# Kernel tuning notes

Measured on AMD Instinct MI355X. Metric: run time of the kernel, lower is better.

The kernel has to match this reference:

```python
import jax, jax.numpy as jnp
import numpy as np
import math

B, L, D = 4, 4096, 1024
PI = math.pi
LN_EPS = 1e-5


def setup_inputs() -> dict:
    key = jax.random.key(0)
    ks = jax.random.split(key, 16)
    s = 1.0 / math.sqrt(D)
    inp = {
        "x": jax.random.normal(ks[0], (B, L, D), dtype=jnp.float32),
        # Linear weights stored as [in, out] (torch W.T)
        "Wk": jax.random.normal(ks[1], (D, D), dtype=jnp.float32) * s,
        "bk": jnp.zeros((D,), dtype=jnp.float32),
        "Wq": jax.random.normal(ks[2], (D, D), dtype=jnp.float32) * s,
        "bq": jnp.zeros((D,), dtype=jnp.float32),
        "Wv": jax.random.normal(ks[3], (D, D), dtype=jnp.float32) * s,
        "bv": jnp.zeros((D,), dtype=jnp.float32),
        "ln_g": jnp.ones((D,), dtype=jnp.float32),
        "ln_b": jnp.zeros((D,), dtype=jnp.float32),
        "Wo": jax.random.normal(ks[4], (D, D), dtype=jnp.float32) * s,
        "bo": jnp.zeros((D,), dtype=jnp.float32),
        "Wg1": jax.random.normal(ks[5], (D, D // 4), dtype=jnp.float32) * s,
        "bg1": jnp.zeros((D // 4,), dtype=jnp.float32),
        "Wg2": jax.random.normal(ks[6], (D // 4, 1), dtype=jnp.float32) * (2.0 / math.sqrt(D)),
        "bg2": jnp.zeros((1,), dtype=jnp.float32),
        "pos_phases": jax.random.normal(ks[7], (L, D), dtype=jnp.float32) * PI,
    }
    return inp


def _layernorm(x, g, b):
    mu = jnp.mean(x, axis=-1, keepdims=True)
    var = jnp.var(x, axis=-1, keepdims=True)
    return (x - mu) * jax.lax.rsqrt(var + LN_EPS) * g + b


def reference(x, Wk, bk, Wq, bq, Wv, bv, ln_g, ln_b, Wo, bo, Wg1, bg1, Wg2, bg2, pos_phases):
    # dropout is identity in eval mode
    key_phases = jnp.tanh(x @ Wk + bk) * PI          # [B,L,D]
    query_phases = jnp.tanh(x @ Wq + bq) * PI        # [B,L,D]
    V = x @ Wv + bv                                   # [B,L,D]

    cos_k, sin_k = jnp.cos(key_phases), jnp.sin(key_phases)
    cos_q, sin_q = jnp.cos(query_phases), jnp.sin(query_phases)

    mem_real = jnp.cumsum(V * cos_k, axis=1)
    mem_imag = jnp.cumsum(V * sin_k, axis=1)
    content_retrieved = mem_real * cos_q + mem_imag * sin_q

    pp = pos_phases[: x.shape[1]]                     # [L,D]
    cos_p, sin_p = jnp.cos(pp), jnp.sin(pp)
    pos_mem_real = jnp.cumsum(V * cos_p, axis=1)
    pos_mem_imag = jnp.cumsum(V * sin_p, axis=1)
    pos_retrieved = pos_mem_real * cos_p + pos_mem_imag * sin_p

    gate = jax.nn.sigmoid(jax.nn.gelu(x @ Wg1 + bg1) @ Wg2 + bg2)  # [B,L,1]
    combined = gate * content_retrieved + (1.0 - gate) * pos_retrieved

    positions = jnp.arange(1, x.shape[1] + 1, dtype=jnp.float32)
    norm = jnp.sqrt(positions)[None, :, None]
    out = _layernorm(combined / norm, ln_g, ln_b) @ Wo + bo
    return x + out
```

## Files before the change

kernel.cpp:

```cpp
#include <hip/hip_runtime.h>
#include <math.h>

#define B_ 4
#define L_ 4096
#define D_ 1024
#define DG_ 256
#define NC_ 128
#define CL_ 32
#define SEGL_ 8
#define NSEG_ 16
#define PI_F 3.14159265358979323846f
#define LN_EPS_F 1e-5f

typedef __attribute__((ext_vector_type(8))) _Float16 f16x8;
typedef __attribute__((ext_vector_type(8))) short s16x8;
typedef __attribute__((ext_vector_type(4))) short s16x4;
typedef __attribute__((ext_vector_type(4))) float f32x4;

__device__ inline short f2h(float f) { return __builtin_bit_cast(short, (_Float16)f); }
__device__ inline float h2f(short s) { return (float)__builtin_bit_cast(_Float16, s); }

__device__ inline float ftanh(float x) {
    float e = __expf(2.0f * x);
    return 1.0f - 2.0f / (e + 1.0f);
}
__device__ inline void fsincos(float x, float* s, float* c) {
    *s = __sinf(x); *c = __cosf(x);
}

__device__ inline void gld16(const void* g, void* l) {
    __builtin_amdgcn_global_load_lds(
        (const __attribute__((address_space(1))) unsigned int*)g,
        (__attribute__((address_space(3))) unsigned int*)l, 16, 0, 0);
}

__global__ __launch_bounds__(256)
void conv_x(const float* __restrict__ x, short* __restrict__ xh, int n8)
{
    int t = blockIdx.x * 256 + threadIdx.x;
    if (t >= n8) return;
    const float4* p = (const float4*)x + (size_t)t * 2;
    float4 a = p[0], b = p[1];
    s16x8 v;
    v[0] = f2h(a.x); v[1] = f2h(a.y); v[2] = f2h(a.z); v[3] = f2h(a.w);
    v[4] = f2h(b.x); v[5] = f2h(b.y); v[6] = f2h(b.z); v[7] = f2h(b.w);
    *(s16x8*)(xh + (size_t)t * 8) = v;
}

__global__ __launch_bounds__(256)
void csp_kernel(const float* __restrict__ PP, short* __restrict__ CSP, int n4)
{
    int t = blockIdx.x * 256 + threadIdx.x;
    if (t >= n4) return;
    f32x4 p = *(const f32x4*)&PP[(size_t)t * 4];
    s16x8 o;
    #pragma unroll
    for (int j = 0; j < 4; ++j) {
        float s, c;
        fsincos(p[j], &s, &c);
        o[2 * j] = f2h(c);
        o[2 * j + 1] = f2h(s);
    }
    *(s16x8*)&CSP[(size_t)t * 8] = o;
}

__global__ __launch_bounds__(256)
void convT(const float* __restrict__ W, short* __restrict__ Th, int N)
{
    __shared__ float tile[64][65];
    const int n0 = blockIdx.x * 64, k0 = blockIdx.y * 64;
    const int t = threadIdx.x;
    const int r = t >> 4, c4 = (t & 15) * 4;

    #pragma unroll
    for (int i = 0; i < 4; ++i) {
        float4 v = *(const float4*)&W[(size_t)(k0 + r + i * 16) * N + n0 + c4];
        tile[r + i * 16][c4 + 0] = v.x;
        tile[r + i * 16][c4 + 1] = v.y;
        tile[r + i * 16][c4 + 2] = v.z;
        tile[r + i * 16][c4 + 3] = v.w;
    }
    __syncthreads();
    #pragma unroll
    for (int i = 0; i < 4; ++i) {
        const int n = r + i * 16;
        s16x4 o;
        o[0] = f2h(tile[c4 + 0][n]);
        o[1] = f2h(tile[c4 + 1][n]);
        o[2] = f2h(tile[c4 + 2][n]);
        o[3] = f2h(tile[c4 + 3][n]);
        *(s16x4*)&Th[(size_t)(n0 + n) * 1024 + k0 + c4] = o;
    }
}

#define BARRIER() __builtin_amdgcn_s_barrier()
#define PRIO1() __builtin_amdgcn_s_setprio(1)
#define PRIO0() __builtin_amdgcn_s_setprio(0)
#define LGKM0() do { asm volatile("s_waitcnt lgkmcnt(0)" ::: "memory"); \
                     __builtin_amdgcn_sched_barrier(0); } while (0)
#define VMC(N) asm volatile("s_waitcnt vmcnt(" #N ")" ::: "memory")

#define DSR(dst, areg, OFS)                                              \
    asm volatile("ds_read_b128 %0, %1 offset:" OFS                       \
                 : "=v"(dst) : "v"(areg))

#define RDA4(areg)                                                       \
    DSR(af[0], areg, "0");    DSR(af[1], areg, "2048");                  \
    DSR(af[2], areg, "4096"); DSR(af[3], areg, "6144");
#define RDA4H(areg)                                                      \
    DSR(af[0], areg, "8192");  DSR(af[1], areg, "10240");                \
    DSR(af[2], areg, "12288"); DSR(af[3], areg, "14336");
#define RDB4(areg, KK)                                                   \
    DSR(bq[0][KK], areg, "0");    DSR(bq[1][KK], areg, "2048");          \
    DSR(bq[2][KK], areg, "4096"); DSR(bq[3][KK], areg, "6144");

#define MF(MG, KK)                                                       \
    _Pragma("unroll") for (int i_ = 0; i_ < 4; ++i_)                     \
    _Pragma("unroll") for (int n_ = 0; n_ < 4; ++n_)                     \
        acc[(MG)*4 + i_][n_] = __builtin_amdgcn_mfma_f32_16x16x32_f16(   \
            af[i_], bq[n_][KK], acc[(MG)*4 + i_][n_], 0, 0, 0);

template<int EPI, typename OT>
__global__ __launch_bounds__(512, 2)
void mgemm256(const short* __restrict__ A, const short* __restrict__ Bt,
              const float* __restrict__ X, OT* __restrict__ out0,
              short* __restrict__ out1, short* __restrict__ out2,
              const float* __restrict__ b0, const float* __restrict__ b1,
              const float* __restrict__ b2, int M, int N, int K)
{
    extern __shared__ char lds[];

    const int tid = threadIdx.x;
    const int w = tid >> 6, l = tid & 63;
    const int wr = w >> 2, wc = w & 3;
    const int fr = l & 15, kb = l >> 4;
    const int bm = blockIdx.x * 256, bn = blockIdx.y * 256;
    const int np = K >> 7;

    const int s = fr & 7;
    const int cK0 = (((s >> 2) & 1) << 6) | (((kb ^ s) & 3) << 4);
    const int aA0 = (wr << 14) + fr * 128 + cK0;
    const int aA1 = aA0 ^ 64;
    const int aB0 = 32768 + ((wc >> 1) << 14) + ((wc & 1) * 64 + fr) * 128 + cK0;
    const int aB1 = aB0 ^ 64;
    const int aA0o = aA0 + 65536, aA1o = aA1 + 65536;
    const int aB0o = aB0 + 65536, aB1o = aB1 + 65536;

    const int p0 = tid * 16;
    const int sr = p0 >> 7;
    const int sc = (p0 & 127) ^ ((sr & 7) << 4);
    const short* gA = A  + (size_t)(bm + sr) * K + (sc >> 1);
    const short* gB = Bt + (size_t)(bn + sr) * K + (sc >> 1);
    char* ldst = lds + (w << 10);
    const size_t q1 = (size_t)64 * K, q2 = 2 * q1, q3 = 3 * q1;

    f32x4 acc[8][4] = {};
    f16x8 af[4];
    f16x8 bq[4][2];

    gld16(gA,      ldst);          gld16(gA + q1, ldst + 8192);
    gld16(gA + q2, ldst + 16384);  gld16(gA + q3, ldst + 24576);
    gld16(gB,      ldst + 32768);  gld16(gB + q1, ldst + 40960);
    gld16(gB + q2, ldst + 49152);  gld16(gB + q3, ldst + 57344);
    gld16(gA +      64, ldst + 65536);
    gld16(gA + q2 + 64, ldst + 65536 + 16384);
    VMC(2);
    BARRIER();

    const short* gAn = gA + 64;
    const short* gBn = gB + 64;

    for (int pp = 0; pp < np; ++pp) {
        const bool nl = (pp + 1 < np);

        RDA4(aA0); RDB4(aB0, 0);
        gld16(gBn,      ldst + 98304);
        gld16(gBn + q1, ldst + 98304 + 8192);
        LGKM0();
        PRIO1(); MF(0, 0); PRIO0();
        RDA4(aA1); RDB4(aB1, 1);
        gld16(gBn + q2, ldst + 98304 + 16384);
        gld16(gBn + q3, ldst + 98304 + 24576);
        gld16(gAn + q1, ldst + 65536 + 8192);
        gld16(gAn + q3, ldst + 65536 + 24576);
        LGKM0();
        PRIO1(); MF(0, 1); PRIO0();
        BARRIER();
        RDA4H(aA0);
        LGKM0();
        PRIO1(); MF(1, 0); PRIO0();
        RDA4H(aA1);
        if (nl) { gld16(gAn + 64, ldst); gld16(gAn + 64 + q2, ldst + 16384); }
        LGKM0();
        PRIO1(); MF(1, 1); PRIO0();
        if (nl) { VMC(2); } else { VMC(0); }
        BARRIER();

        RDA4(aA0o); RDB4(aB0o, 0);
        if (nl) {
            gld16(gBn +      64, ldst + 32768);
            gld16(gBn + q1 + 64, ldst + 40960);
        }
        LGKM0();
        PRIO1(); MF(0, 0); PRIO0();
        RDA4(aA1o); RDB4(aB1o, 1);
        if (nl) {
            gld16(gBn + q2 + 64, ldst + 49152);
            gld16(gBn + q3 + 64, ldst + 57344);
            gld16(gAn + q1 + 64, ldst + 8192);
            gld16(gAn + q3 + 64, ldst + 24576);
        }
        LGKM0();
        PRIO1(); MF(0, 1); PRIO0();
        BARRIER();
        RDA4H(aA0o);
        LGKM0();
        PRIO1(); MF(1, 0); PRIO0();
        RDA4H(aA1o);
        if (nl) { gld16(gAn + 128, ldst + 65536); gld16(gAn + 128 + q2, ldst + 65536 + 16384); }
        LGKM0();
        PRIO1(); MF(1, 1); PRIO0();
        if (nl) {
            VMC(2);
            BARRIER();
        }
        gAn += 128; gBn += 128;
    }

    if constexpr (EPI == 4) {
        short* op; const float* bp; bool dt;
        if (bn < 1024)      { op = (short*)out0; bp = b0; dt = true;  }
        else if (bn < 2048) { op = out1;         bp = b1; dt = true;  }
        else                { op = out2;         bp = b2; dt = false; }
        const int cb = bn & 1023;
        float bc[4];
        #pragma unroll
        for (int nf = 0; nf < 4; ++nf) bc[nf] = bp[cb + wc * 64 + nf * 16 + fr];
        #pragma unroll
        for (int mf = 0; mf < 8; ++mf)
            #pragma unroll
            for (int rr = 0; rr < 4; ++rr) {
                const int row = bm + wr * 128 + mf * 16 + kb * 4 + rr;
                #pragma unroll
                for (int nf = 0; nf < 4; ++nf) {
                    const int cc = cb + wc * 64 + nf * 16 + fr;
                    float c = acc[mf][nf][rr] + bc[nf];
                    if (dt) c = ftanh(c) * PI_F;
                    op[(size_t)row * 1024 + cc] = f2h(c);
                }
            }
    } else {
        float bc[4];
        #pragma unroll
        for (int nf = 0; nf < 4; ++nf) bc[nf] = b0[bn + wc * 64 + nf * 16 + fr];
        #pragma unroll
        for (int mf = 0; mf < 8; ++mf)
            #pragma unroll
            for (int rr = 0; rr < 4; ++rr) {
                const int row = bm + wr * 128 + mf * 16 + kb * 4 + rr;
                #pragma unroll
                for (int nf = 0; nf < 4; ++nf) {
                    const int col = bn + wc * 64 + nf * 16 + fr;
                    float c = acc[mf][nf][rr] + bc[nf] + X[(size_t)row * N + col];
                    ((float*)out0)[(size_t)row * N + col] = c;
                }
            }
    }
}

#define RDAF(areg)                                                       \
    DSR(af[0], areg, "0");    DSR(af[1], areg, "2048");                  \
    DSR(af[2], areg, "4096"); DSR(af[3], areg, "6144");
#define RDBF(areg)                                                       \
    DSR(bqs[0], areg, "0");    DSR(bqs[1], areg, "2048");                \
    DSR(bqs[2], areg, "4096"); DSR(bqs[3], areg, "6144");

#define MF16()                                                           \
    _Pragma("unroll") for (int i_ = 0; i_ < 4; ++i_)                     \
    _Pragma("unroll") for (int n_ = 0; n_ < 4; ++n_)                     \
        acc[i_][n_] = __builtin_amdgcn_mfma_f32_16x16x32_f16(            \
            af[i_], bqs[n_], acc[i_][n_], 0, 0, 0);

template<int EPI>
__global__ __launch_bounds__(256, 2)
void gemm128(const short* __restrict__ A, const short* __restrict__ Bt,
             const float* __restrict__ b0, const float* __restrict__ wg2p,
             float* __restrict__ gatep, int M, int N, int K)
{
    extern __shared__ char lds[];

    const int tid = threadIdx.x;
    const int w = tid >> 6, l = tid & 63;
    const int wr = w >> 1, wc = w & 1;
    const int fr = l & 15, kb = l >> 4;
    const int bm = blockIdx.x * 128, bn = blockIdx.y * 128;

    const int s = fr & 7;
    const int cK0 = (((s >> 2) & 1) << 6) | (((kb ^ s) & 3) << 4);
    const int aA0e = (wr * 64 + fr) * 128 + cK0;
    const int aA1e = aA0e ^ 64;
    const int aB0e = 16384 + (wc * 64 + fr) * 128 + cK0;
    const int aB1e = aB0e ^ 64;
    const int aA0o = aA0e + 32768, aA1o = aA1e + 32768;
    const int aB0o = aB0e + 32768, aB1o = aB1e + 32768;

    const int p16 = tid * 16;
    const int sr = p16 >> 7;
    const int sc = (p16 & 127) ^ ((sr & 7) << 4);
    const short* gA = A  + (size_t)(bm + sr) * K + (sc >> 1);
    const short* gB = Bt + (size_t)(bn + sr) * K + (sc >> 1);
    char* ldA = lds + (w << 10);
    const size_t r32 = (size_t)32 * K;

    f32x4 acc[4][4] = {};
    f16x8 af[4], bqs[4];

    #pragma unroll
    for (int i = 0; i < 4; ++i) gld16(gA + i * r32, ldA + i * 4096);
    #pragma unroll
    for (int i = 0; i < 4; ++i) gld16(gB + i * r32, ldA + 16384 + i * 4096);
    VMC(0);
    BARRIER();

    const short* gAt = gA;
    const short* gBt = gB;
    const int np = K >> 7;

    for (int pp = 0; pp < np; ++pp) {
        const bool nl = (pp + 1 < np);

        RDAF(aA0e); RDBF(aB0e);
        #pragma unroll
        for (int i = 0; i < 4; ++i) gld16(gAt + 64 + i * r32, ldA + 32768 + i * 4096);
        LGKM0();
        PRIO1(); MF16(); PRIO0();
        RDAF(aA1e); RDBF(aB1e);
        #pragma unroll
        for (int i = 0; i < 4; ++i) gld16(gBt + 64 + i * r32, ldA + 49152 + i * 4096);
        LGKM0();
        PRIO1(); MF16(); PRIO0();
        VMC(0);
        BARRIER();

        RDAF(aA0o); RDBF(aB0o);
        if (nl) {
            #pragma unroll
            for (int i = 0; i < 4; ++i) gld16(gAt + 128 + i * r32, ldA + i * 4096);
        }
        LGKM0();
        PRIO1(); MF16(); PRIO0();
        RDAF(aA1o); RDBF(aB1o);
        if (nl) {
            #pragma unroll
            for (int i = 0; i < 4; ++i) gld16(gBt + 128 + i * r32, ldA + 16384 + i * 4096);
        }
        LGKM0();
        PRIO1(); MF16(); PRIO0();
        if (nl) {
            VMC(0);
            BARRIER();
        }
        gAt += 128; gBt += 128;
    }

    float bg[4], wg[4];
    #pragma unroll
    for (int nf = 0; nf < 4; ++nf) {
        const int cl = bn + wc * 64 + nf * 16 + fr;
        bg[nf] = b0[cl];
        wg[nf] = wg2p[cl];
    }
    #pragma unroll
    for (int mf = 0; mf < 4; ++mf)
        #pragma unroll
        for (int rr = 0; rr < 4; ++rr) {
            const int row = bm + wr * 64 + mf * 16 + kb * 4 + rr;
            float part = 0.f;
            #pragma unroll
            for (int nf = 0; nf < 4; ++nf) {
                float c = acc[mf][nf][rr] + bg[nf];
                float tt = 0.7978845608028654f * (c + 0.044715f * c * c * c);
                float g = 0.5f * c * (1.0f + ftanh(tt));
                part += g * wg[nf];
            }
            part += __shfl_xor(part, 1);
            part += __shfl_xor(part, 2);
            part += __shfl_xor(part, 4);
            part += __shfl_xor(part, 8);
            if (fr == 0) atomicAdd(&gatep[row], part);
        }
}

__global__ __launch_bounds__(256)
void passA(const short* __restrict__ V, const short* __restrict__ KP,
           const short* __restrict__ CSP, f32x4* __restrict__ SI)
{
    const int bid = blockIdx.x;
    const int b = bid >> 7, c = bid & 127;
    const int d0 = threadIdx.x * 4;

    f32x4 cr = {}, ci = {}, pr = {}, pi = {};
    const size_t base  = ((size_t)b * L_ + (size_t)c * CL_) * D_ + d0;
    const size_t pcs   = ((size_t)c * CL_ * D_ + d0) * 2;
    for (int ll = 0; ll < CL_; ++ll) {
        s16x4 v4  = *(const s16x4*)&V [base + (size_t)ll * D_];
        s16x4 kp4 = *(const s16x4*)&KP[base + (size_t)ll * D_];
        s16x8 c8  = *(const s16x8*)&CSP[pcs + (size_t)ll * (D_ * 2)];
        #pragma unroll
        for (int j = 0; j < 4; ++j) {
            float v = h2f(v4[j]);
            float sk, ck;
            fsincos(h2f(kp4[j]), &sk, &ck);
            float cp = h2f(c8[2 * j]), sp = h2f(c8[2 * j + 1]);
            cr[j] += v * ck; ci[j] += v * sk;
            pr[j] += v * cp; pi[j] += v * sp;
        }
    }
    const size_t sidx = ((size_t)bid << 10) + d0;
    #pragma unroll
    for (int j = 0; j < 4; ++j) {
        f32x4 o = { cr[j], ci[j], pr[j], pi[j] };
        SI[sidx + j] = o;
    }
}

__global__ __launch_bounds__(256)
void passB1(f32x4* __restrict__ SI, f32x4* __restrict__ STS)
{
    const int seg = blockIdx.x & (NSEG_ - 1);
    const int t = (blockIdx.x >> 4) * 256 + threadIdx.x;
    const int b = t >> 10, d = t & 1023;
    f32x4 run = {};
    #pragma unroll
    for (int i = 0; i < SEGL_; ++i) {
        const int c = seg * SEGL_ + i;
        const size_t idx = ((size_t)(b * NC_ + c) << 10) + d;
        f32x4 v = SI[idx];
        SI[idx] = run;
        run += v;
    }
    STS[((size_t)(b * NSEG_ + seg) << 10) + d] = run;
}

__global__ __launch_bounds__(256)
void passB2(f32x4* __restrict__ STS)
{
    const int t = blockIdx.x * 256 + threadIdx.x;
    const int b = t >> 10, d = t & 1023;
    f32x4 run = {};
    #pragma unroll
    for (int seg = 0; seg < NSEG_; ++seg) {
        const size_t idx = ((size_t)(b * NSEG_ + seg) << 10) + d;
        f32x4 v = STS[idx];
        STS[idx] = run;
        run += v;
    }
}

__global__ __launch_bounds__(256)
void passC(const short* __restrict__ V, const short* KP,
           const short* __restrict__ QP, const short* __restrict__ CSP,
           const float* __restrict__ gatep, const float* __restrict__ bg2,
           const f32x4* __restrict__ SI, const f32x4* __restrict__ STS,
           const float* __restrict__ ln_g, const float* __restrict__ ln_b,
           short* Yb)
{
    const int bid = blockIdx.x;
    const int b = bid >> 7, c = bid & 127;
    const int d0 = threadIdx.x * 4;

    const size_t sidx = ((size_t)bid << 10) + d0;
    const size_t tidx = ((size_t)(b * NSEG_ + (c >> 3)) << 10) + d0;
    f32x4 cr, ci, pr, pi;
    #pragma unroll
    for (int j = 0; j < 4; ++j) {
        f32x4 s0 = SI[sidx + j] + STS[tidx + j];
        cr[j] = s0[0]; ci[j] = s0[1]; pr[j] = s0[2]; pi[j] = s0[3];
    }
    const f32x4 g_ln = *(const f32x4*)&ln_g[d0];
    const f32x4 b_ln = *(const f32x4*)&ln_b[d0];
    const float bg2v = bg2[0];

    __shared__ float2 lred[2][4];
    const int wid = threadIdx.x >> 6;
    const int lane = threadIdx.x & 63;

    const int lbase = c * CL_;
    size_t off = ((size_t)b * L_ + lbase) * D_ + d0;
    size_t cso = ((size_t)lbase * D_ + d0) * 2;
    s16x4 v4  = *(const s16x4*)&V [off];
    s16x4 kp4 = *(const s16x4*)&KP[off];
    s16x4 qp4 = *(const s16x4*)&QP[off];
    s16x8 c8  = *(const s16x8*)&CSP[cso];
    float gpre = gatep[b * L_ + lbase];

    for (int l0 = 0; l0 < CL_; ++l0) {
        const int ll = lbase + l0;
        const size_t offn = off + D_;
        s16x4 v4n = v4, kp4n = kp4, qp4n = qp4;
        s16x8 c8n = c8; float gpn = gpre;
        if (l0 + 1 < CL_) {
            v4n  = *(const s16x4*)&V [offn];
            kp4n = *(const s16x4*)&KP[offn];
            qp4n = *(const s16x4*)&QP[offn];
            c8n  = *(const s16x8*)&CSP[cso + D_ * 2];
            gpn  = gatep[b * L_ + ll + 1];
        }

        const float gv = 1.0f / (1.0f + __expf(-(gpre + bg2v)));
        const float rs_pos = rsqrtf((float)(ll + 1));

        f32x4 u;
        #pragma unroll
        for (int j = 0; j < 4; ++j) {
            float v = h2f(v4[j]);
            float sk, ck, sq, cq;
            fsincos(h2f(kp4[j]), &sk, &ck);
            fsincos(h2f(qp4[j]), &sq, &cq);
            float cp = h2f(c8[2 * j]), sp = h2f(c8[2 * j + 1]);
            cr[j] += v * ck; ci[j] += v * sk;
            pr[j] += v * cp; pi[j] += v * sp;
            float content = cr[j] * cq + ci[j] * sq;
            float posr    = pr[j] * cp + pi[j] * sp;
            u[j] = (gv * content + (1.0f - gv) * posr) * rs_pos;
        }

        float sm  = u[0] + u[1] + u[2] + u[3];
        float s2 = u[0]*u[0] + u[1]*u[1] + u[2]*u[2] + u[3]*u[3];
        #pragma unroll
        for (int o = 32; o; o >>= 1) {
            sm += __shfl_down(sm, o);
            s2 += __shfl_down(s2, o);
        }
        const int pb = l0 & 1;
        if (lane == 0) lred[pb][wid] = make_float2(sm, s2);
        asm volatile("s_waitcnt lgkmcnt(0)" ::: "memory");
        __builtin_amdgcn_s_barrier();
        float ts  = lred[pb][0].x + lred[pb][1].x + lred[pb][2].x + lred[pb][3].x;
        float ts2 = lred[pb][0].y + lred[pb][1].y + lred[pb][2].y + lred[pb][3].y;
        const float mu  = ts * (1.0f / D_);
        const float var = ts2 * (1.0f / D_) - mu * mu;
        const float rsv = rsqrtf(var + LN_EPS_F);
        s16x4 yo;
        #pragma unroll
        for (int j = 0; j < 4; ++j)
            yo[j] = f2h((u[j] - mu) * rsv * g_ln[j] + b_ln[j]);
        *(s16x4*)&Yb[off] = yo;

        off = offn; cso += D_ * 2;
        v4 = v4n; kp4 = kp4n; qp4 = qp4n; c8 = c8n; gpre = gpn;
    }
}

extern "C" void kernel_launch(void* const* d_in, const int* in_sizes, int n_in,
                              void* d_out, int out_size, void* d_ws, size_t ws_size,
                              hipStream_t stream)
{
    const float* x    = (const float*)d_in[0];
    const float* Wk   = (const float*)d_in[1];
    const float* bk   = (const float*)d_in[2];
    const float* Wq   = (const float*)d_in[3];
    const float* bq   = (const float*)d_in[4];
    const float* Wv   = (const float*)d_in[5];
    const float* bv   = (const float*)d_in[6];
    const float* ln_g = (const float*)d_in[7];
    const float* ln_b = (const float*)d_in[8];
    const float* Wo   = (const float*)d_in[9];
    const float* bo   = (const float*)d_in[10];
    const float* Wg1  = (const float*)d_in[11];
    const float* bg1  = (const float*)d_in[12];
    const float* Wg2  = (const float*)d_in[13];
    const float* bg2  = (const float*)d_in[14];
    const float* PP   = (const float*)d_in[15];

    float* out = (float*)d_out;

    const size_t BLD   = (size_t)B_ * L_ * D_;
    const size_t SZ_X  = BLD * 2;
    const size_t SZ_R1 = (size_t)B_ * L_ * DG_ * 2;
    const size_t SZ_G1 = (size_t)D_ * DG_ * 2;
    const size_t SZ_GT = (size_t)B_ * L_ * 4;
    const size_t NEED  = SZ_X + SZ_R1 + SZ_G1 + 3 * SZ_X + SZ_GT;
    if (ws_size < NEED) {
        hipMemcpyAsync(d_out, d_in[0], BLD * sizeof(float),
                       hipMemcpyDeviceToDevice, stream);
        return;
    }

    char* wsb = (char*)d_ws;
    short* xh   = (short*)(wsb);
    char*  r1   = wsb + SZ_X;
    short* Wcat = (short*)r1;
    short* Wg1T = (short*)(r1 + SZ_R1);
    short* KP   = (short*)(r1 + SZ_R1 + SZ_G1);
    short* QP   = (short*)((char*)KP + SZ_X);
    short* V    = (short*)((char*)QP + SZ_X);
    float* gatep = (float*)((char*)V + SZ_X);
    short* WtO  = (short*)(wsb);
    f32x4* SI   = (f32x4*)(wsb + 2097152);
    short* CSP  = (short*)(wsb + 2097152 + 8388608);
    f32x4* STS  = (f32x4*)(wsb + 2097152 + 8388608 + 16777216);
    short* Yb   = KP;

    const int M = B_ * L_;
    dim3 blk(256);

    conv_x<<<(int)(BLD / 8 / 256), blk, 0, stream>>>(x, xh, (int)(BLD / 8));
    dim3 gT(D_ / 64, 16);
    dim3 gTg(DG_ / 64, 16);
    convT<<<gT, blk, 0, stream>>>(Wk, Wcat + (size_t)0 * D_ * D_, D_);
    convT<<<gT, blk, 0, stream>>>(Wq, Wcat + (size_t)1 * D_ * D_, D_);
    convT<<<gT, blk, 0, stream>>>(Wv, Wcat + (size_t)2 * D_ * D_, D_);
    convT<<<gTg, blk, 0, stream>>>(Wg1, Wg1T, DG_);
    hipMemsetAsync(gatep, 0, SZ_GT, stream);

    dim3 gQKV(M / 256, 3072 / 256);
    hipLaunchKernelGGL((mgemm256<4, short>), gQKV, dim3(512), 131072, stream,
                       xh, Wcat, nullptr, KP, QP, V, bk, bq, bv, M, 3072, D_);
    dim3 gH(M / 128, DG_ / 128);
    hipLaunchKernelGGL((gemm128<5>), gH, blk, 65536, stream,
                       xh, Wg1T, bg1, Wg2, gatep, M, DG_, D_);

    convT<<<gT, blk, 0, stream>>>(Wo, WtO, D_);
    csp_kernel<<<(int)((size_t)L_ * D_ / 4 / 256), blk, 0, stream>>>(
        PP, CSP, (int)((size_t)L_ * D_ / 4));

    passA<<<B_ * NC_, blk, 0, stream>>>(V, KP, CSP, SI);
    passB1<<<(B_ * D_ / 256) * NSEG_, blk, 0, stream>>>(SI, STS);
    passB2<<<B_ * D_ / 256, blk, 0, stream>>>(STS);
    passC<<<B_ * NC_, blk, 0, stream>>>(V, KP, QP, CSP, gatep, bg2, SI, STS,
                                        ln_g, ln_b, Yb);

    dim3 gO(M / 256, D_ / 256);
    hipLaunchKernelGGL((mgemm256<3, float>), gO, dim3(512), 131072, stream,
                       Yb, WtO, x, out, nullptr, nullptr, bo, nullptr, nullptr,
                       M, D_, D_);
}
```

Measured before the change: 282.7 us.

## Halve scan chunk length, make passC one wave per row, simplify GEMM prefetch

Scan chunk length drops from 32 to 16 rows, doubling the number of chunks and segments. passC now gives each wavefront a whole row chunk with 16 columns per lane, so the LayerNorm reduction uses only wave shuffles and drops the per-row LDS exchange and block barrier. The mgemm256 main loop is restructured to issue full A/B tile prefetches per half-step and wait for all loads (VMC(0)) before a single barrier, removing a mid-step barrier but shortening the in-flight prefetch window. Workspace buffers are relocated to fit the larger SI array; the per-lane register footprint in passC grows substantially.

Result: no change. 282.6 us, median of 2 (-0.0%).

```diff
diff --git a/kernel.cpp b/kernel.cpp
--- a/kernel.cpp
+++ b/kernel.cpp
@@ -5,10 +5,10 @@
 #define L_ 4096
 #define D_ 1024
 #define DG_ 256
-#define NC_ 128
-#define CL_ 32
+#define NC_ 256
+#define CL_ 16
 #define SEGL_ 8
-#define NSEG_ 16
+#define NSEG_ 32
 #define PI_F 3.14159265358979323846f
 #define LN_EPS_F 1e-5f
 
@@ -162,9 +162,7 @@
     gld16(gA + q2, ldst + 16384);  gld16(gA + q3, ldst + 24576);
     gld16(gB,      ldst + 32768);  gld16(gB + q1, ldst + 40960);
     gld16(gB + q2, ldst + 49152);  gld16(gB + q3, ldst + 57344);
-    gld16(gA +      64, ldst + 65536);
-    gld16(gA + q2 + 64, ldst + 65536 + 16384);
-    VMC(2);
+    VMC(0);
     BARRIER();
 
     const short* gAn = gA + 64;
@@ -174,54 +172,46 @@
         const bool nl = (pp + 1 < np);
 
         RDA4(aA0); RDB4(aB0, 0);
-        gld16(gBn,      ldst + 98304);
-        gld16(gBn + q1, ldst + 98304 + 8192);
+        gld16(gBn,      ldst + 98304);         gld16(gBn + q1, ldst + 98304 + 8192);
+        gld16(gBn + q2, ldst + 98304 + 16384); gld16(gBn + q3, ldst + 98304 + 24576);
         LGKM0();
         PRIO1(); MF(0, 0); PRIO0();
         RDA4(aA1); RDB4(aB1, 1);
-        gld16(gBn + q2, ldst + 98304 + 16384);
-        gld16(gBn + q3, ldst + 98304 + 24576);
-        gld16(gAn + q1, ldst + 65536 + 8192);
-        gld16(gAn + q3, ldst + 65536 + 24576);
+        gld16(gAn,      ldst + 65536);         gld16(gAn + q1, ldst + 65536 + 8192);
+        gld16(gAn + q2, ldst + 65536 + 16384); gld16(gAn + q3, ldst + 65536 + 24576);
         LGKM0();
         PRIO1(); MF(0, 1); PRIO0();
-        BARRIER();
         RDA4H(aA0);
         LGKM0();
         PRIO1(); MF(1, 0); PRIO0();
         RDA4H(aA1);
-        if (nl) { gld16(gAn + 64, ldst); gld16(gAn + 64 + q2, ldst + 16384); }
         LGKM0();
         PRIO1(); MF(1, 1); PRIO0();
-        if (nl) { VMC(2); } else { VMC(0); }
+        VMC(0);
         BARRIER();
 
         RDA4(aA0o); RDB4(aB0o, 0);
         if (nl) {
-            gld16(gBn +      64, ldst + 32768);
-            gld16(gBn + q1 + 64, ldst + 40960);
+            gld16(gBn +      64, ldst + 32768); gld16(gBn + q1 + 64, ldst + 40960);
+            gld16(gBn + q2 + 64, ldst + 49152); gld16(gBn + q3 + 64, ldst + 57344);
         }
         LGKM0();
         PRIO1(); MF(0, 0); PRIO0();
         RDA4(aA1o); RDB4(aB1o, 1);
         if (nl) {
-            gld16(gBn + q2 + 64, ldst + 49152);
-            gld16(gBn + q3 + 64, ldst + 57344);
-            gld16(gAn + q1 + 64, ldst + 8192);
-            gld16(gAn + q3 + 64, ldst + 24576);
+            gld16(gAn +      64, ldst);         gld16(gAn + q1 + 64, ldst + 8192);
+            gld16(gAn + q2 + 64, ldst + 16384); gld16(gAn + q3 + 64, ldst + 24576);
         }
         LGKM0();
         PRIO1(); MF(0, 1); PRIO0();
-        BARRIER();
         RDA4H(aA0o);
         LGKM0();
         PRIO1(); MF(1, 0); PRIO0();
         RDA4H(aA1o);
-        if (nl) { gld16(gAn + 128, ldst + 65536); gld16(gAn + 128 + q2, ldst + 65536 + 16384); }
         LGKM0();
         PRIO1(); MF(1, 1); PRIO0();
         if (nl) {
-            VMC(2);
+            VMC(0);
             BARRIER();
         }
         gAn += 128; gBn += 128;
@@ -396,12 +386,12 @@
            const short* __restrict__ CSP, f32x4* __restrict__ SI)
 {
     const int bid = blockIdx.x;
-    const int b = bid >> 7, c = bid & 127;
+    const int b = bid >> 8, c = bid & 255;
     const int d0 = threadIdx.x * 4;
 
     f32x4 cr = {}, ci = {}, pr = {}, pi = {};
-    const size_t base  = ((size_t)b * L_ + (size_t)c * CL_) * D_ + d0;
-    const size_t pcs   = ((size_t)c * CL_ * D_ + d0) * 2;
+    const size_t base = ((size_t)b * L_ + (size_t)c * CL_) * D_ + d0;
+    const size_t pcs  = ((size_t)c * CL_ * D_ + d0) * 2;
     for (int ll = 0; ll < CL_; ++ll) {
         s16x4 v4  = *(const s16x4*)&V [base + (size_t)ll * D_];
         s16x4 kp4 = *(const s16x4*)&KP[base + (size_t)ll * D_];
@@ -428,7 +418,7 @@
 void passB1(f32x4* __restrict__ SI, f32x4* __restrict__ STS)
 {
     const int seg = blockIdx.x & (NSEG_ - 1);
-    const int t = (blockIdx.x >> 4) * 256 + threadIdx.x;
+    const int t = (blockIdx.x >> 5) * 256 + threadIdx.x;
     const int b = t >> 10, d = t & 1023;
     f32x4 run = {};
     #pragma unroll
@@ -465,90 +455,107 @@
            const float* __restrict__ ln_g, const float* __restrict__ ln_b,
            short* Yb)
 {
-    const int bid = blockIdx.x;
-    const int b = bid >> 7, c = bid & 127;
-    const int d0 = threadIdx.x * 4;
-
-    const size_t sidx = ((size_t)bid << 10) + d0;
+    const int w = threadIdx.x >> 6, lane = threadIdx.x & 63;
+    const int gw = blockIdx.x * 4 + w;
+    const int b = gw >> 8, c = gw & 255;
+    const int d0 = lane * 16;
+
+    const size_t sidx = ((size_t)gw << 10) + d0;
     const size_t tidx = ((size_t)(b * NSEG_ + (c >> 3)) << 10) + d0;
-    f32x4 cr, ci, pr, pi;
-    #pragma unroll
-    for (int j = 0; j < 4; ++j) {
+    float cr[16], ci[16], pr[16], pi[16];
+    #pragma unroll
+    for (int j = 0; j < 16; ++j) {
         f32x4 s0 = SI[sidx + j] + STS[tidx + j];
         cr[j] = s0[0]; ci[j] = s0[1]; pr[j] = s0[2]; pi[j] = s0[3];
     }
-    const f32x4 g_ln = *(const f32x4*)&ln_g[d0];
-    const f32x4 b_ln = *(const f32x4*)&ln_b[d0];
+    float gl[16], bl[16];
+    #pragma unroll
+    for (int j = 0; j < 16; ++j) { gl[j] = ln_g[d0 + j]; bl[j] = ln_b[d0 + j]; }
     const float bg2v = bg2[0];
-
-    __shared__ float2 lred[2][4];
-    const int wid = threadIdx.x >> 6;
-    const int lane = threadIdx.x & 63;
 
     const int lbase = c * CL_;
     size_t off = ((size_t)b * L_ + lbase) * D_ + d0;
     size_t cso = ((size_t)lbase * D_ + d0) * 2;
-    s16x4 v4  = *(const s16x4*)&V [off];
-    s16x4 kp4 = *(const s16x4*)&KP[off];
-    s16x4 qp4 = *(const s16x4*)&QP[off];
-    s16x8 c8  = *(const s16x8*)&CSP[cso];
+
+    s16x8 v8a, v8b, k8a, k8b, q8a, q8b, c8a, c8b, c8c, c8d;
+    v8a = *(const s16x8*)&V [off];      v8b = *(const s16x8*)&V [off + 8];
+    k8a = *(const s16x8*)&KP[off];      k8b = *(const s16x8*)&KP[off + 8];
+    q8a = *(const s16x8*)&QP[off];      q8b = *(const s16x8*)&QP[off + 8];
+    c8a = *(const s16x8*)&CSP[cso];     c8b = *(const s16x8*)&CSP[cso + 8];
+    c8c = *(const s16x8*)&CSP[cso + 16];c8d = *(const s16x8*)&CSP[cso + 24];
     float gpre = gatep[b * L_ + lbase];
 
     for (int l0 = 0; l0 < CL_; ++l0) {
         const int ll = lbase + l0;
         const size_t offn = off + D_;
-        s16x4 v4n = v4, kp4n = kp4, qp4n = qp4;
-        s16x8 c8n = c8; float gpn = gpre;
+        const size_t cson = cso + D_ * 2;
+        s16x8 v8an = v8a, v8bn = v8b, k8an = k8a, k8bn = k8b;
+        s16x8 q8an = q8a, q8bn = q8b, c8an = c8a, c8bn = c8b, c8cn = c8c, c8dn = c8d;
+        float gpn = gpre;
         if (l0 + 1 < CL_) {
-            v4n  = *(const s16x4*)&V [offn];
-            kp4n = *(const s16x4*)&KP[offn];
-            qp4n = *(const s16x4*)&QP[offn];
-            c8n  = *(const s16x8*)&CSP[cso + D_ * 2];
+            v8an = *(const s16x8*)&V [offn];      v8bn = *(const s16x8*)&V [offn + 8];
+            k8an = *(const s16x8*)&KP[offn];      k8bn = *(const s16x8*)&KP[offn + 8];
+            q8an = *(const s16x8*)&QP[offn];      q8bn = *(const s16x8*)&QP[offn + 8];
+            c8an = *(const s16x8*)&CSP[cson];     c8bn = *(const s16x8*)&CSP[cson + 8];
+            c8cn = *(const s16x8*)&CSP[cson + 16];c8dn = *(const s16x8*)&CSP[cson + 24];
             gpn  = gatep[b * L_ + ll + 1];
         }
 
         const float gv = 1.0f / (1.0f + __expf(-(gpre + bg2v)));
         const float rs_pos = rsqrtf((float)(ll + 1));
 
-        f32x4 u;
-        #pragma unroll
-        for (int j = 0; j < 4; ++j) {
-            float v = h2f(v4[j]);
+        float u[16];
+        float sm = 0.f, s2 = 0.f;
+        #pragma unroll
+        for (int j = 0; j < 16; ++j) {
+            const short vs = (j < 8) ? v8a[j & 7] : v8b[j & 7];
+            const short ks = (j < 8) ? k8a[j & 7] : k8b[j & 7];
+            const short qs = (j < 8) ? q8a[j & 7] : q8b[j & 7];
+            const int cj = 2 * j;
+            const short cps = (cj < 8) ? c8a[cj & 7]
+                             : (cj < 16) ? c8b[cj & 7]
+                             : (cj < 24) ? c8c[cj & 7] : c8d[cj & 7];
+            const short sps = (cj + 1 < 8) ? c8a[(cj + 1) & 7]
+                             : (cj + 1 < 16) ? c8b[(cj + 1) & 7]
+                             : (cj + 1 < 24) ? c8c[(cj + 1) & 7] : c8d[(cj + 1) & 7];
+            float v = h2f(vs);
             float sk, ck, sq, cq;
-            fsincos(h2f(kp4[j]), &sk, &ck);
-            fsincos(h2f(qp4[j]), &sq, &cq);
-            float cp = h2f(c8[2 * j]), sp = h2f(c8[2 * j + 1]);
+            fsincos(h2f(ks), &sk, &ck);
+            fsincos(h2f(qs), &sq, &cq);
+            float cp = h2f(cps), sp = h2f(sps);
             cr[j] += v * ck; ci[j] += v * sk;
             pr[j] += v * cp; pi[j] += v * sp;
             float content = cr[j] * cq + ci[j] * sq;
             float posr    = pr[j] * cp + pi[j] * sp;
             u[j] = (gv * content + (1.0f - gv) * posr) * rs_pos;
-        }
-
-        float sm  = u[0] + u[1] + u[2] + u[3];
-        float s2 = u[0]*u[0] + u[1]*u[1] + u[2]*u[2] + u[3]*u[3];
+            sm += u[j]; s2 += u[j] * u[j];
+        }
+
         #pragma unroll
         for (int o = 32; o; o >>= 1) {
             sm += __shfl_down(sm, o);
             s2 += __shfl_down(s2, o);
         }
-        const int pb = l0 & 1;
-        if (lane == 0) lred[pb][wid] = make_float2(sm, s2);
-        asm volatile("s_waitcnt lgkmcnt(0)" ::: "memory");
-        __builtin_amdgcn_s_barrier();
-        float ts  = lred[pb][0].x + lred[pb][1].x + lred[pb][2].x + lred[pb][3].x;
-        float ts2 = lred[pb][0].y + lred[pb][1].y + lred[pb][2].y + lred[pb][3].y;
-        const float mu  = ts * (1.0f / D_);
-        const float var = ts2 * (1.0f / D_) - mu * mu;
+        sm = __shfl(sm, 0);
+        s2 = __shfl(s2, 0);
+        const float mu  = sm * (1.0f / D_);
+        const float var = s2 * (1.0f / D_) - mu * mu;
         const float rsv = rsqrtf(var + LN_EPS_F);
-        s16x4 yo;
-        #pragma unroll
-        for (int j = 0; j < 4; ++j)
-            yo[j] = f2h((u[j] - mu) * rsv * g_ln[j] + b_ln[j]);
-        *(s16x4*)&Yb[off] = yo;
-
-        off = offn; cso += D_ * 2;
-        v4 = v4n; kp4 = kp4n; qp4 = qp4n; c8 = c8n; gpre = gpn;
+        s16x8 yo0, yo1;
+        #pragma unroll
+        for (int j = 0; j < 8; ++j)
+            yo0[j] = f2h((u[j] - mu) * rsv * gl[j] + bl[j]);
+        #pragma unroll
+        for (int j = 0; j < 8; ++j)
+            yo1[j] = f2h((u[8 + j] - mu) * rsv * gl[8 + j] + bl[8 + j]);
+        *(s16x8*)&Yb[off] = yo0;
+        *(s16x8*)&Yb[off + 8] = yo1;
+
+        off = offn; cso = cson;
+        v8a = v8an; v8b = v8bn; k8a = k8an; k8b = k8bn;
+        q8a = q8an; q8b = q8bn;
+        c8a = c8an; c8b = c8bn; c8c = c8cn; c8d = c8dn;
+        gpre = gpn;
     }
 }
 
@@ -596,10 +603,10 @@
     short* QP   = (short*)((char*)KP + SZ_X);
     short* V    = (short*)((char*)QP + SZ_X);
     float* gatep = (float*)((char*)V + SZ_X);
-    short* WtO  = (short*)(wsb);
-    f32x4* SI   = (f32x4*)(wsb + 2097152);
-    short* CSP  = (short*)(wsb + 2097152 + 8388608);
-    f32x4* STS  = (f32x4*)(wsb + 2097152 + 8388608 + 16777216);
+    f32x4* SI   = (f32x4*)(wsb);
+    short* CSP  = (short*)(wsb + 16777216);
+    short* WtO  = (short*)r1;
+    f32x4* STS  = (f32x4*)(r1 + 2097152);
     short* Yb   = KP;
 
     const int M = B_ * L_;
@@ -628,8 +635,8 @@
     passA<<<B_ * NC_, blk, 0, stream>>>(V, KP, CSP, SI);
     passB1<<<(B_ * D_ / 256) * NSEG_, blk, 0, stream>>>(SI, STS);
     passB2<<<B_ * D_ / 256, blk, 0, stream>>>(STS);
-    passC<<<B_ * NC_, blk, 0, stream>>>(V, KP, QP, CSP, gatep, bg2, SI, STS,
-                                        ln_g, ln_b, Yb);
+    passC<<<B_ * NC_ / 4, blk, 0, stream>>>(V, KP, QP, CSP, gatep, bg2, SI, STS,
+                                            ln_g, ln_b, Yb);
 
     dim3 gO(M / 256, D_ / 256);
     hipLaunchKernelGGL((mgemm256<3, float>), gO, dim3(512), 131072, stream,
```
